# Kernel optimization log

Measured on AMD Instinct MI355X. Metric: run time of the kernel, lower is better.

Reference implementation:

```python
import jax, jax.numpy as jnp
import numpy as np

N = 4096; E = 65536; IN = 512; H = 256; QD = 256; NH = 8; HD = QD // NH
OUT = 10; L = 2; CT = 50


def _ln(x, g, b, eps=1e-5):
    mu = x.mean(-1, keepdims=True)
    var = ((x - mu) ** 2).mean(-1, keepdims=True)
    return (x - mu) * jax.lax.rsqrt(var + eps) * g + b


def _forward(x, edge_index, cell_types, Wi, bi, Wq, bq, Wk, bk, Wv, bv, Bc, cemb,
             Win, bin_p, Wo, bo, Wm1, bm1, Wm2, bm2, Wm3, bm3, ln_g, ln_b,
             Wc1, bc1, Wc2, bc2):
    src, tgt = edge_index[0], edge_index[1]
    h = jax.nn.relu(x @ Wi + bi)                      # [N, H] input projection
    # graph connectivity scattered into a dense mask (as in _create_attention_mask)
    mask = jnp.zeros((N, N), jnp.float32).at[src, tgt].set(1.0)
    for l in range(L):
        res = h
        Q = h @ Wq[l] + bq[l]                         # [N, QD]
        K = h @ Wk[l] + bk[l]
        V = h @ Wv[l] + bv[l]
        Q = Q @ Bc[l]                                 # biological constraint
        K = K @ Bc[l].T
        ce = cemb[l][cell_types]                      # [N, QD] cell-type embedding
        Q = Q + 0.1 * ce
        K = K + 0.1 * ce
        # dense graph-masked attention (entanglement matrix), applied to V
        scores = (Q @ K.T) / float(np.sqrt(QD))      # [N, N]
        scores = jnp.where(mask == 0.0, -1e9, scores)
        attn = jax.nn.softmax(scores, axis=-1)
        graph_att = attn @ V                          # [N, QD]
        # nn.MultiheadAttention(Q, K, V) entanglement layer (eval mode)
        q = (Q @ Win[l, :, :QD] + bin_p[l, :QD]).reshape(N, NH, HD)
        k = (K @ Win[l, :, QD:2 * QD] + bin_p[l, QD:2 * QD]).reshape(N, NH, HD)
        v = (V @ Win[l, :, 2 * QD:] + bin_p[l, 2 * QD:]).reshape(N, NH, HD)
        w = jax.nn.softmax(jnp.einsum('nhd,mhd->hnm', q, k) / float(np.sqrt(HD)), axis=-1)
        mha = jnp.einsum('hnm,mhd->nhd', w, v).reshape(N, QD) @ Wo[l] + bo[l]
        # edge gather -> message MLP -> scatter-add (PyG aggr='add', x_i=target, x_j=source)
        # quantum slot of the concat is zeros, so only the first 2H rows of Wm1 contribute
        m = jnp.concatenate([h[tgt], h[src]], axis=-1) @ Wm1[l, :2 * H] + bm1[l]
        m = jax.nn.relu(m)
        m = jax.nn.relu(m @ Wm2[l] + bm2[l])
        m = m @ Wm3[l] + bm3[l]                       # [E, H]
        agg = jax.ops.segment_sum(m, tgt, num_segments=N)
        h = _ln(res + agg + mha + graph_att, ln_g[l], ln_b[l])
    # graph-level readout: mean || max pooling -> classifier (hidden*2 -> hidden -> out)
    pooled = jnp.concatenate([h.mean(0), h.max(0)], axis=-1)   # [2H]
    z = jax.nn.relu(pooled @ Wc1 + bc1)
    return z @ Wc2 + bc2                              # [OUT]


def setup_inputs():
    ks = jax.random.split(jax.random.key(0), 40)
    s = 0.05
    p = lambda i, shape: jax.random.normal(ks[i], shape, jnp.float32) * s
    z = lambda shape: jnp.zeros(shape, jnp.float32)
    return {
        'x': jax.random.normal(ks[0], (N, IN), jnp.float32),
        'edge_index': jax.random.randint(ks[1], (2, E), 0, N),
        'cell_types': jax.random.randint(ks[2], (N,), 0, CT),
        'Wi': p(3, (IN, H)), 'bi': z((H,)),
        'Wq': p(4, (L, H, QD)), 'bq': z((L, QD)),
        'Wk': p(5, (L, H, QD)), 'bk': z((L, QD)),
        'Wv': p(6, (L, H, QD)), 'bv': z((L, QD)),
        'Bc': p(7, (L, QD, QD)),
        'cemb': p(8, (L, CT, QD)),
        'Win': p(9, (L, QD, 3 * QD)), 'bin_p': z((L, 3 * QD)),
        'Wo': p(10, (L, QD, QD)), 'bo': z((L, QD)),
        'Wm1': p(11, (L, 2 * H + QD, QD)), 'bm1': z((L, QD)),
        'Wm2': p(12, (L, QD, QD)), 'bm2': z((L, QD)),
        'Wm3': p(13, (L, QD, H)), 'bm3': z((L, H)),
        'ln_g': jnp.ones((L, H), jnp.float32), 'ln_b': z((L, H)),
        'Wc1': p(14, (2 * H, H)), 'bc1': z((H,)),
        'Wc2': p(15, (H, OUT)), 'bc2': z((OUT,)),
    }


def reference(x, edge_index, cell_types, Wi, bi, Wq, bq, Wk, bk, Wv, bv, Bc, cemb,
              Win, bin_p, Wo, bo, Wm1, bm1, Wm2, bm2, Wm3, bm3, ln_g, ln_b,
              Wc1, bc1, Wc2, bc2):
    return _forward(x, edge_index, cell_types, Wi, bi, Wq, bq, Wk, bk, Wv, bv, Bc, cemb,
                    Win, bin_p, Wo, bo, Wm1, bm1, Wm2, bm2, Wm3, bm3, ln_g, ln_b,
                    Wc1, bc1, Wc2, bc2)
```

## Files before the change

kernel.cpp:

```cpp
#include <hip/hip_runtime.h>
#include <hip/hip_bf16.h>

#define N_NODES 4096
#define E_EDGES 65536
#define IN_F    512
#define H_F     256
#define QD      256
#define NHEAD   8
#define HD      32
#define OUT_F   10
#define L_LAYERS 2
#define CT_N    50

enum { FLAG_RELU = 1, FLAG_ACCUM = 2, FLAG_WF32 = 4, FLAG_WB16 = 8 };

typedef __attribute__((ext_vector_type(8))) __bf16 bf16x8;
typedef __attribute__((ext_vector_type(4))) float f32x4;

union PU { bf16x8 v; __hip_bfloat16 h[8]; };

template<int BM, int BN, bool EDGE>
__global__ __launch_bounds__(256) void gemm_mfma(
    const __hip_bfloat16* __restrict__ A, int lda,
    const __hip_bfloat16* __restrict__ B, int ldb,
    float* __restrict__ Cf, __hip_bfloat16* __restrict__ Cb, int ldc,
    int K,
    const float* __restrict__ bias, const float* __restrict__ rowscale,
    const float* __restrict__ extra, const int* __restrict__ eidx, float esc,
    const int* __restrict__ tgtp, const int* __restrict__ srcp,
    const float* __restrict__ kbias,
    int flags)
{
    constexpr int WM = BM / 2, WN = BN / 2, MT = WM / 16, NT = WN / 16;
    constexpr int LDT = 40;
    __shared__ alignas(16) __hip_bfloat16 As[BM * LDT];
    __shared__ alignas(16) __hip_bfloat16 Bs[BN * LDT];

    const int tid = threadIdx.x;
    const int w = tid >> 6, lane = tid & 63, l16 = lane & 15, quad = lane >> 4;
    const int wm = w >> 1, wn = w & 1;
    const int bm = blockIdx.y * BM, bn = blockIdx.x * BN;

    f32x4 acc[MT][NT];
    #pragma unroll
    for (int i = 0; i < MT; ++i)
        #pragma unroll
        for (int j = 0; j < NT; ++j)
            #pragma unroll
            for (int r = 0; r < 4; ++r) acc[i][j][r] = 0.f;

    for (int k0 = 0; k0 < K; k0 += 32) {
        #pragma unroll
        for (int f = tid; f < BM * 4; f += 256) {
            int r = f >> 2, sg = f & 3;
            if (EDGE) {
                int i = bm + r;
                int tg = tgtp[i], sr = srcp[i];
                PU z1, z2, o;
                z1.v = *reinterpret_cast<const bf16x8*>(A + (size_t)tg * 512 + k0 + sg * 8);
                z2.v = *reinterpret_cast<const bf16x8*>(A + (size_t)sr * 512 + 256 + k0 + sg * 8);
                float4 b0 = *reinterpret_cast<const float4*>(kbias + k0 + sg * 8);
                float4 b1 = *reinterpret_cast<const float4*>(kbias + k0 + sg * 8 + 4);
                float bb[8] = {b0.x, b0.y, b0.z, b0.w, b1.x, b1.y, b1.z, b1.w};
                #pragma unroll
                for (int j = 0; j < 8; ++j) {
                    float v = __bfloat162float(z1.h[j]) + __bfloat162float(z2.h[j]) + bb[j];
                    o.h[j] = __float2bfloat16(fmaxf(v, 0.f));
                }
                *reinterpret_cast<bf16x8*>(&As[r * LDT + sg * 8]) = o.v;
            } else {
                *reinterpret_cast<uint4*>(&As[r * LDT + sg * 8]) =
                    *reinterpret_cast<const uint4*>(A + (size_t)(bm + r) * lda + k0 + sg * 8);
            }
        }
        #pragma unroll
        for (int f = tid; f < BN * 4; f += 256) {
            int r = f >> 2, sg = f & 3;
            *reinterpret_cast<uint4*>(&Bs[r * LDT + sg * 8]) =
                *reinterpret_cast<const uint4*>(B + (size_t)(bn + r) * ldb + k0 + sg * 8);
        }
        __syncthreads();
        bf16x8 af[MT], bfr[NT];
        #pragma unroll
        for (int mt = 0; mt < MT; ++mt)
            af[mt] = *reinterpret_cast<const bf16x8*>(&As[(wm * WM + mt * 16 + l16) * LDT + quad * 8]);
        #pragma unroll
        for (int nt = 0; nt < NT; ++nt)
            bfr[nt] = *reinterpret_cast<const bf16x8*>(&Bs[(wn * WN + nt * 16 + l16) * LDT + quad * 8]);
        #pragma unroll
        for (int mt = 0; mt < MT; ++mt)
            #pragma unroll
            for (int nt = 0; nt < NT; ++nt)
                acc[mt][nt] = __builtin_amdgcn_mfma_f32_16x16x32_bf16(af[mt], bfr[nt], acc[mt][nt], 0, 0, 0);
        __syncthreads();
    }

    #pragma unroll
    for (int mt = 0; mt < MT; ++mt) {
        #pragma unroll
        for (int nt = 0; nt < NT; ++nt) {
            int col = bn + wn * WN + nt * 16 + l16;
            #pragma unroll
            for (int r = 0; r < 4; ++r) {
                int row = bm + wm * WM + mt * 16 + quad * 4 + r;
                float v = acc[mt][nt][r];
                if (bias) {
                    float bv = bias[col];
                    if (rowscale) bv *= rowscale[row];
                    v += bv;
                }
                if (extra) v += esc * extra[(size_t)eidx[row] * QD + col];
                if (flags & FLAG_RELU) v = fmaxf(v, 0.f);
                size_t off = (size_t)row * ldc + col;
                if (flags & FLAG_ACCUM)     Cf[off] += v;
                else if (flags & FLAG_WF32) Cf[off] = v;
                if (flags & FLAG_WB16)      Cb[off] = __float2bfloat16(v);
            }
        }
    }
}

struct GSet { const __hip_bfloat16* A; int lda; const __hip_bfloat16* B;
              const float* bias; const float* rowscale;
              const float* extra; float esc; float cscale;
              __hip_bfloat16* C; float* Cf; int vtout; };
struct GPack3 { GSet s[3]; };

__global__ __launch_bounds__(256) void gemm_b3(GPack3 p, const int* __restrict__ eidx)
{
    GSet g = p.s[blockIdx.z];
    constexpr int LDT = 40;
    __shared__ alignas(16) __hip_bfloat16 As[64 * LDT];
    __shared__ alignas(16) __hip_bfloat16 Bs[64 * LDT];

    const int tid = threadIdx.x;
    const int w = tid >> 6, lane = tid & 63, l16 = lane & 15, quad = lane >> 4;
    const int wm = w >> 1, wn = w & 1;
    const int bm = blockIdx.y * 64, bn = blockIdx.x * 64;

    f32x4 acc[2][2];
    #pragma unroll
    for (int i = 0; i < 2; ++i)
        #pragma unroll
        for (int j = 0; j < 2; ++j)
            #pragma unroll
            for (int r = 0; r < 4; ++r) acc[i][j][r] = 0.f;

    for (int k0 = 0; k0 < 256; k0 += 32) {
        #pragma unroll
        for (int f = tid; f < 256; f += 256) {
            int r = f >> 2, sg = f & 3;
            *reinterpret_cast<uint4*>(&As[r * LDT + sg * 8]) =
                *reinterpret_cast<const uint4*>(g.A + (size_t)(bm + r) * g.lda + k0 + sg * 8);
            *reinterpret_cast<uint4*>(&Bs[r * LDT + sg * 8]) =
                *reinterpret_cast<const uint4*>(g.B + (size_t)(bn + r) * 256 + k0 + sg * 8);
        }
        __syncthreads();
        bf16x8 af[2], bfr[2];
        #pragma unroll
        for (int mt = 0; mt < 2; ++mt)
            af[mt] = *reinterpret_cast<const bf16x8*>(&As[(wm * 32 + mt * 16 + l16) * LDT + quad * 8]);
        #pragma unroll
        for (int nt = 0; nt < 2; ++nt)
            bfr[nt] = *reinterpret_cast<const bf16x8*>(&Bs[(wn * 32 + nt * 16 + l16) * LDT + quad * 8]);
        #pragma unroll
        for (int mt = 0; mt < 2; ++mt)
            #pragma unroll
            for (int nt = 0; nt < 2; ++nt)
                acc[mt][nt] = __builtin_amdgcn_mfma_f32_16x16x32_bf16(af[mt], bfr[nt], acc[mt][nt], 0, 0, 0);
        __syncthreads();
    }

    #pragma unroll
    for (int mt = 0; mt < 2; ++mt) {
        #pragma unroll
        for (int nt = 0; nt < 2; ++nt) {
            int col = bn + wn * 32 + nt * 16 + l16;
            #pragma unroll
            for (int r = 0; r < 4; ++r) {
                int row = bm + wm * 32 + mt * 16 + quad * 4 + r;
                float v = acc[mt][nt][r];
                if (g.bias) {
                    float bv = g.bias[col];
                    if (g.rowscale) bv *= g.rowscale[row];
                    v += bv;
                }
                if (g.extra) v += g.esc * g.extra[(size_t)eidx[row] * QD + col];
                v *= g.cscale;
                if (g.vtout)
                    g.C[(size_t)col * 4096 + row] = __float2bfloat16(v);
                else if (g.Cf)
                    g.Cf[(size_t)row * 256 + col] = v;
                else
                    g.C[(size_t)row * 256 + col] = __float2bfloat16(v);
            }
        }
    }
}

__global__ __launch_bounds__(256) void mha_flash5(
    const __hip_bfloat16* __restrict__ Qm,
    const __hip_bfloat16* __restrict__ Km,
    const __hip_bfloat16* __restrict__ Vt, __hip_bfloat16* __restrict__ Out)
{
    const int hh = blockIdx.y;
    const int tid = threadIdx.x;
    const int w = tid >> 6, lane = tid & 63, l16 = lane & 15, quad = lane >> 4;
    const int qb = blockIdx.x * 32;

    __shared__ float Osh[3][2][64][8];
    __shared__ float Lsh[3][2][16];

    const bf16x8 aq0 = *reinterpret_cast<const bf16x8*>(
        Qm + (size_t)(qb + l16) * 256 + hh * 32 + quad * 8);
    const bf16x8 aq1 = *reinterpret_cast<const bf16x8*>(
        Qm + (size_t)(qb + 16 + l16) * 256 + hh * 32 + quad * 8);
    const __hip_bfloat16* vb0 = Vt + (size_t)(hh * 32 + l16) * 4096;
    const __hip_bfloat16* vb1 = vb0 + (size_t)16 * 4096;
    const int rowoff = (l16 >> 2) * 8 + (l16 & 3);
    const f32x4 zero = {0.f, 0.f, 0.f, 0.f};

    f32x4 o00 = zero, o01 = zero, o10 = zero, o11 = zero;
    float l0 = 0.f, l1 = 0.f;

    const int kstart = w * 1024;
    for (int kt = 0; kt < 16; ++kt) {
        const int kbase = kstart + kt * 64;
        bf16x8 kf[4];
        #pragma unroll
        for (int c = 0; c < 2; ++c)
            #pragma unroll
            for (int st = 0; st < 2; ++st)
                kf[c * 2 + st] = *reinterpret_cast<const bf16x8*>(
                    Km + (size_t)(kbase + c * 32 + st * 4 + rowoff) * 256 + hh * 32 + quad * 8);
        bf16x8 v00 = *reinterpret_cast<const bf16x8*>(vb0 + kbase + quad * 8);
        bf16x8 v01 = *reinterpret_cast<const bf16x8*>(vb1 + kbase + quad * 8);
        bf16x8 v10 = *reinterpret_cast<const bf16x8*>(vb0 + kbase + 32 + quad * 8);
        bf16x8 v11 = *reinterpret_cast<const bf16x8*>(vb1 + kbase + 32 + quad * 8);

        {
            f32x4 s[4];
            #pragma unroll
            for (int i = 0; i < 4; ++i)
                s[i] = __builtin_amdgcn_mfma_f32_16x16x32_bf16(kf[i], aq0, zero, 0, 0, 0);
            PU p0, p1;
            float ls = 0.f;
            #pragma unroll
            for (int r = 0; r < 4; ++r) {
                float e0 = exp2f(s[0][r]), e1 = exp2f(s[1][r]);
                float e2 = exp2f(s[2][r]), e3 = exp2f(s[3][r]);
                ls += (e0 + e1) + (e2 + e3);
                p0.h[r] = __float2bfloat16(e0); p0.h[4 + r] = __float2bfloat16(e1);
                p1.h[r] = __float2bfloat16(e2); p1.h[4 + r] = __float2bfloat16(e3);
            }
            l0 += ls;
            o00 = __builtin_amdgcn_mfma_f32_16x16x32_bf16(v00, p0.v, o00, 0, 0, 0);
            o01 = __builtin_amdgcn_mfma_f32_16x16x32_bf16(v01, p0.v, o01, 0, 0, 0);
            o00 = __builtin_amdgcn_mfma_f32_16x16x32_bf16(v10, p1.v, o00, 0, 0, 0);
            o01 = __builtin_amdgcn_mfma_f32_16x16x32_bf16(v11, p1.v, o01, 0, 0, 0);
        }
        {
            f32x4 s[4];
            #pragma unroll
            for (int i = 0; i < 4; ++i)
                s[i] = __builtin_amdgcn_mfma_f32_16x16x32_bf16(kf[i], aq1, zero, 0, 0, 0);
            PU p0, p1;
            float ls = 0.f;
            #pragma unroll
            for (int r = 0; r < 4; ++r) {
                float e0 = exp2f(s[0][r]), e1 = exp2f(s[1][r]);
                float e2 = exp2f(s[2][r]), e3 = exp2f(s[3][r]);
                ls += (e0 + e1) + (e2 + e3);
                p0.h[r] = __float2bfloat16(e0); p0.h[4 + r] = __float2bfloat16(e1);
                p1.h[r] = __float2bfloat16(e2); p1.h[4 + r] = __float2bfloat16(e3);
            }
            l1 += ls;
            o10 = __builtin_amdgcn_mfma_f32_16x16x32_bf16(v00, p0.v, o10, 0, 0, 0);
            o11 = __builtin_amdgcn_mfma_f32_16x16x32_bf16(v01, p0.v, o11, 0, 0, 0);
            o10 = __builtin_amdgcn_mfma_f32_16x16x32_bf16(v10, p1.v, o10, 0, 0, 0);
            o11 = __builtin_amdgcn_mfma_f32_16x16x32_bf16(v11, p1.v, o11, 0, 0, 0);
        }
    }

    l0 += __shfl_xor(l0, 16); l0 += __shfl_xor(l0, 32);
    l1 += __shfl_xor(l1, 16); l1 += __shfl_xor(l1, 32);

    if (w > 0) {
        #pragma unroll
        for (int r = 0; r < 4; ++r) {
            Osh[w - 1][0][lane][r]     = o00[r];
            Osh[w - 1][0][lane][4 + r] = o01[r];
            Osh[w - 1][1][lane][r]     = o10[r];
            Osh[w - 1][1][lane][4 + r] = o11[r];
        }
        if (quad == 0) { Lsh[w - 1][0][l16] = l0; Lsh[w - 1][1][l16] = l1; }
    }
    __syncthreads();
    if (w == 0) {
        #pragma unroll
        for (int ww = 0; ww < 3; ++ww) {
            #pragma unroll
            for (int r = 0; r < 4; ++r) {
                o00[r] += Osh[ww][0][lane][r];
                o01[r] += Osh[ww][0][lane][4 + r];
                o10[r] += Osh[ww][1][lane][r];
                o11[r] += Osh[ww][1][lane][4 + r];
            }
            l0 += Lsh[ww][0][l16];
            l1 += Lsh[ww][1][l16];
        }
        {
            float inv = 1.f / l0;
            __hip_bfloat16* dst = Out + (size_t)(qb + l16) * 256 + hh * 32;
            #pragma unroll
            for (int r = 0; r < 4; ++r) {
                dst[quad * 4 + r]      = __float2bfloat16(o00[r] * inv);
                dst[16 + quad * 4 + r] = __float2bfloat16(o01[r] * inv);
            }
        }
        {
            float inv = 1.f / l1;
            __hip_bfloat16* dst = Out + (size_t)(qb + 16 + l16) * 256 + hh * 32;
            #pragma unroll
            for (int r = 0; r < 4; ++r) {
                dst[quad * 4 + r]      = __float2bfloat16(o10[r] * inv);
                dst[16 + quad * 4 + r] = __float2bfloat16(o11[r] * inv);
            }
        }
    }
}

__global__ __launch_bounds__(256) void build_mask(const int* __restrict__ src,
                                                  const int* __restrict__ tgt,
                                                  unsigned* __restrict__ mb)
{
    int e = blockIdx.x * 256 + threadIdx.x;
    if (e >= E_EDGES) return;
    atomicOr(mb + (size_t)src[e] * (N_NODES / 32) + (tgt[e] >> 5), 1u << (tgt[e] & 31));
}

__global__ __launch_bounds__(256) void csr_count(const int* __restrict__ tgt, int* __restrict__ cnt)
{
    int e = blockIdx.x * 256 + threadIdx.x;
    if (e < E_EDGES) atomicAdd(&cnt[tgt[e]], 1);
}

__global__ __launch_bounds__(1024) void csr_scan(const int* __restrict__ cnt, int* __restrict__ off,
                                                 int* __restrict__ cursor, float* __restrict__ degf)
{
    __shared__ int sh[1024];
    int t = threadIdx.x;
    int base = t * 4;
    int c0 = cnt[base], c1 = cnt[base + 1], c2 = cnt[base + 2], c3 = cnt[base + 3];
    int sum = c0 + c1 + c2 + c3;
    sh[t] = sum; __syncthreads();
    for (int d = 1; d < 1024; d <<= 1) {
        int v = (t >= d) ? sh[t - d] : 0;
        __syncthreads();
        sh[t] += v;
        __syncthreads();
    }
    int excl = sh[t] - sum;
    int o0 = excl, o1 = excl + c0, o2 = o1 + c1, o3 = o2 + c2;
    off[base] = o0; off[base + 1] = o1; off[base + 2] = o2; off[base + 3] = o3;
    cursor[base] = o0; cursor[base + 1] = o1; cursor[base + 2] = o2; cursor[base + 3] = o3;
    degf[base] = (float)c0; degf[base + 1] = (float)c1;
    degf[base + 2] = (float)c2; degf[base + 3] = (float)c3;
    if (t == 1023) off[4096] = sh[t];
}

__global__ __launch_bounds__(256) void csr_fill(const int* __restrict__ src, const int* __restrict__ tgt,
                                                int* __restrict__ cursor,
                                                int* __restrict__ srcp, int* __restrict__ tgtp)
{
    int e = blockIdx.x * 256 + threadIdx.x;
    if (e >= E_EDGES) return;
    int t = tgt[e];
    int pos = atomicAdd(&cursor[t], 1);
    srcp[pos] = src[e];
    tgtp[pos] = t;
}

__global__ __launch_bounds__(256) void seg_sum(const int* __restrict__ off,
                                               const __hip_bfloat16* __restrict__ M2,
                                               __hip_bfloat16* __restrict__ A3)
{
    int n = blockIdx.x, t = threadIdx.x;
    int b0 = off[n], b1 = off[n + 1];
    float s = 0.f;
    for (int i = b0; i < b1; ++i)
        s += __bfloat162float(M2[(size_t)i * 256 + t]);
    A3[(size_t)n * 256 + t] = __float2bfloat16(s);
}

__global__ __launch_bounds__(256) void sparse_attn(
    const __hip_bfloat16* __restrict__ Q, const __hip_bfloat16* __restrict__ K,
    const __hip_bfloat16* __restrict__ V, int vld,
    const unsigned* __restrict__ maskb, float* __restrict__ outb)
{
    int i = blockIdx.x, t = threadIdx.x;
    __shared__ float qsh[256];
    __shared__ int   nb[1024];
    __shared__ float sc[1024];
    __shared__ int   cnt;
    __shared__ float red[4];
    __shared__ float smax, ssum;
    if (t == 0) cnt = 0;
    qsh[t] = __bfloat162float(Q[(size_t)i * 256 + t]);
    __syncthreads();
    if (t < 128) {
        unsigned wv = maskb[(size_t)i * 128 + t];
        while (wv) {
            int b = __ffs(wv) - 1; wv &= wv - 1;
            int p = atomicAdd(&cnt, 1);
            nb[p] = t * 32 + b;
        }
    }
    __syncthreads();
    int deg = cnt;
    int wid = t >> 6, lane = t & 63;
    if (deg > 0) {
        for (int n = wid; n < deg; n += 4) {
            union { uint2 u; __hip_bfloat16 h[4]; } kv;
            kv.u = *reinterpret_cast<const uint2*>(K + (size_t)nb[n] * 256 + lane * 4);
            float s = qsh[lane*4+0] * __bfloat162float(kv.h[0]) + qsh[lane*4+1] * __bfloat162float(kv.h[1])
                    + qsh[lane*4+2] * __bfloat162float(kv.h[2]) + qsh[lane*4+3] * __bfloat162float(kv.h[3]);
            #pragma unroll
            for (int off = 32; off; off >>= 1) s += __shfl_xor(s, off);
            if (lane == 0) sc[n] = s * 0.0625f;
        }
        __syncthreads();
        float m = -3.4e38f;
        for (int n = t; n < deg; n += 256) m = fmaxf(m, sc[n]);
        #pragma unroll
        for (int off = 32; off; off >>= 1) m = fmaxf(m, __shfl_xor(m, off));
        if (lane == 0) red[wid] = m;
        __syncthreads();
        if (t == 0) smax = fmaxf(fmaxf(red[0], red[1]), fmaxf(red[2], red[3]));
        __syncthreads();
        float ls = 0.f;
        for (int n = t; n < deg; n += 256) { float e = __expf(sc[n] - smax); sc[n] = e; ls += e; }
        #pragma unroll
        for (int off = 32; off; off >>= 1) ls += __shfl_xor(ls, off);
        if (lane == 0) red[wid] = ls;
        __syncthreads();
        if (t == 0) ssum = red[0] + red[1] + red[2] + red[3];
        __syncthreads();
        float inv = 1.f / ssum;
        float o = 0.f;
        for (int n = 0; n < deg; ++n)
            o += sc[n] * __bfloat162float(V[(size_t)nb[n] * vld + t]);
        outb[(size_t)i * 256 + t] = o * inv;
    } else {
        float o = 0.f;
        for (int j = 0; j < N_NODES; ++j) o += __bfloat162float(V[(size_t)j * vld + t]);
        outb[(size_t)i * 256 + t] = o * (1.f / N_NODES);
    }
}

__global__ __launch_bounds__(256) void ln_kernel(float* __restrict__ h, __hip_bfloat16* __restrict__ h16,
                                                 const float* __restrict__ a1,
                                                 const float* __restrict__ a2,
                                                 const float* __restrict__ a3,
                                                 const float* __restrict__ g, const float* __restrict__ b)
{
    int row = blockIdx.x, t = threadIdx.x;
    __shared__ float red[256];
    size_t off = ((size_t)row << 8) + t;
    float v = h[off] + a1[off] + a2[off] + a3[off];
    red[t] = v; __syncthreads();
    for (int s = 128; s > 0; s >>= 1) { if (t < s) red[t] += red[t + s]; __syncthreads(); }
    float mu = red[0] * (1.f / 256.f); __syncthreads();
    float d = v - mu;
    red[t] = d * d; __syncthreads();
    for (int s = 128; s > 0; s >>= 1) { if (t < s) red[t] += red[t + s]; __syncthreads(); }
    float var = red[0] * (1.f / 256.f);
    float r = d * rsqrtf(var + 1e-5f) * g[t] + b[t];
    h[off] = r;
    h16[off] = __float2bfloat16(r);
}

__global__ __launch_bounds__(256) void colpool(const float* __restrict__ h, float* __restrict__ p)
{
    int c = blockIdx.x, t = threadIdx.x;
    __shared__ float rs[256], rm[256];
    float s = 0.f, m = -3.4e38f;
    for (int row = t; row < N_NODES; row += 256) {
        float v = h[((size_t)row << 8) + c];
        s += v; m = fmaxf(m, v);
    }
    rs[t] = s; rm[t] = m; __syncthreads();
    for (int st = 128; st > 0; st >>= 1) {
        if (t < st) { rs[t] += rs[t + st]; rm[t] = fmaxf(rm[t], rm[t + st]); }
        __syncthreads();
    }
    if (t == 0) { p[c] = rs[0] * (1.f / N_NODES); p[256 + c] = rm[0]; }
}

__global__ __launch_bounds__(256) void classifier(const float* __restrict__ pooled,
                                                  const float* __restrict__ Wc1, const float* __restrict__ bc1,
                                                  const float* __restrict__ Wc2, const float* __restrict__ bc2,
                                                  float* __restrict__ out)
{
    __shared__ float p[512];
    __shared__ float z[256];
    int t = threadIdx.x;
    p[t] = pooled[t]; p[256 + t] = pooled[256 + t];
    __syncthreads();
    float s = bc1[t];
    for (int k = 0; k < 512; ++k) s = fmaf(p[k], Wc1[k * 256 + t], s);
    z[t] = fmaxf(s, 0.f);
    __syncthreads();
    if (t < OUT_F) {
        float o = bc2[t];
        for (int j = 0; j < 256; ++j) o = fmaf(z[j], Wc2[j * OUT_F + t], o);
        out[t] = o;
    }
}

__global__ void concat_qkv_bias(const float* __restrict__ bq, const float* __restrict__ bk,
                                const float* __restrict__ bv, float* __restrict__ out)
{
    int l = blockIdx.x, t = threadIdx.x;
    float v = (t < 256) ? bq[l * 256 + t] : (t < 512) ? bk[l * 256 + t - 256] : bv[l * 256 + t - 512];
    out[l * 768 + t] = v;
}

struct CDesc { const float* s; __hip_bfloat16* d; int total; };
struct CPack { CDesc d[4]; };
__global__ __launch_bounds__(256) void convert_copy(CPack p)
{
    CDesc c = p.d[blockIdx.y];
    for (int i = blockIdx.x * 256 + threadIdx.x; i < c.total; i += gridDim.x * 256)
        c.d[i] = __float2bfloat16(c.s[i]);
}
struct TDesc { const float* s; __hip_bfloat16* d; int K, N, sld; };
struct TPack { TDesc d[25]; };
__global__ __launch_bounds__(256) void convert_t32(TPack p)
{
    TDesc c = p.d[blockIdx.z];
    int k0 = blockIdx.x * 32, n0 = blockIdx.y * 32;
    if (k0 >= c.K || n0 >= c.N) return;
    __shared__ float t[32][33];
    int tr = threadIdx.x >> 5, tc = threadIdx.x & 31;
    #pragma unroll
    for (int rr = 0; rr < 32; rr += 8)
        t[tc][tr + rr] = c.s[(size_t)(k0 + tr + rr) * c.sld + n0 + tc];
    __syncthreads();
    #pragma unroll
    for (int rr = 0; rr < 32; rr += 8)
        c.d[(size_t)(n0 + tr + rr) * c.K + k0 + tc] = __float2bfloat16(t[tr + rr][tc]);
}

template<int BM, int BN>
static void launchG(const __hip_bfloat16* A, int lda, const __hip_bfloat16* B, int ldb,
                    float* Cf, __hip_bfloat16* Cb, int ldc, int M, int Nn, int K,
                    const float* bias, const float* rowscale,
                    const float* extra, const int* eidx, float esc,
                    int flags, hipStream_t s)
{
    dim3 g(Nn / BN, M / BM);
    gemm_mfma<BM, BN, false><<<g, 256, 0, s>>>(A, lda, B, ldb, Cf, Cb, ldc, K, bias, rowscale,
                                               extra, eidx, esc, nullptr, nullptr, nullptr, flags);
}

extern "C" void kernel_launch(void* const* d_in, const int* in_sizes, int n_in,
                              void* d_out, int out_size, void* d_ws, size_t ws_size,
                              hipStream_t stream)
{
    const float* x    = (const float*)d_in[0];
    const int*   ei   = (const int*)d_in[1];
    const int*   ct   = (const int*)d_in[2];
    const float* Wi   = (const float*)d_in[3];
    const float* bi   = (const float*)d_in[4];
    const float* Wq   = (const float*)d_in[5];
    const float* bq   = (const float*)d_in[6];
    const float* Wk   = (const float*)d_in[7];
    const float* bk   = (const float*)d_in[8];
    const float* Wv   = (const float*)d_in[9];
    const float* bv   = (const float*)d_in[10];
    const float* Bc   = (const float*)d_in[11];
    const float* cemb = (const float*)d_in[12];
    const float* Win  = (const float*)d_in[13];
    const float* binp = (const float*)d_in[14];
    const float* Wo   = (const float*)d_in[15];
    const float* bo   = (const float*)d_in[16];
    const float* Wm1  = (const float*)d_in[17];
    const float* bm1  = (const float*)d_in[18];
    const float* Wm2  = (const float*)d_in[19];
    const float* bm2  = (const float*)d_in[20];
    const float* Wm3  = (const float*)d_in[21];
    const float* bm3  = (const float*)d_in[22];
    const float* lng  = (const float*)d_in[23];
    const float* lnb  = (const float*)d_in[24];
    const float* Wc1  = (const float*)d_in[25];
    const float* bc1  = (const float*)d_in[26];
    const float* Wc2  = (const float*)d_in[27];
    const float* bc2  = (const float*)d_in[28];

    const int* src = ei;
    const int* tgt = ei + E_EDGES;

    char* wp = (char*)d_ws;
    auto alloc = [&](size_t bytes) { char* r = wp; wp += (bytes + 255) & ~(size_t)255; return r; };
    const size_t NH = (size_t)N_NODES * 256;
    float* h      = (float*)alloc(NH * 4);
    float* a1     = (float*)alloc(NH * 4);
    float* a2     = (float*)alloc(NH * 4);
    float* a3     = (float*)alloc(NH * 4);
    float* pooled = (float*)alloc(512 * 4);
    float* bqkv   = (float*)alloc(2 * 768 * 4);
    float* degf   = (float*)alloc(N_NODES * 4);
    __hip_bfloat16* x16 = (__hip_bfloat16*)alloc((size_t)N_NODES * 512 * 2);
    __hip_bfloat16* h16 = (__hip_bfloat16*)alloc(NH * 2);
    __hip_bfloat16* Ta  = (__hip_bfloat16*)alloc((size_t)N_NODES * 768 * 2);
    __hip_bfloat16* Qb  = (__hip_bfloat16*)alloc(NH * 2);
    __hip_bfloat16* Kb  = (__hip_bfloat16*)alloc(NH * 2);
    __hip_bfloat16* Tq  = (__hip_bfloat16*)alloc(NH * 2);
    __hip_bfloat16* Tk  = (__hip_bfloat16*)alloc(NH * 2);
    __hip_bfloat16* Vt  = (__hip_bfloat16*)alloc(NH * 2);
    __hip_bfloat16* Z12 = (__hip_bfloat16*)alloc((size_t)N_NODES * 512 * 2);
    __hip_bfloat16* M216= (__hip_bfloat16*)alloc((size_t)E_EDGES * 256 * 2);
    __hip_bfloat16* A3  = (__hip_bfloat16*)alloc(NH * 2);
    __hip_bfloat16* Wi_t= (__hip_bfloat16*)alloc((size_t)256 * 512 * 2);
    __hip_bfloat16* WB[2][10];
    for (int l = 0; l < 2; ++l) {
        WB[l][0] = (__hip_bfloat16*)alloc(3 * 65536 * 2);
        for (int m = 1; m < 7; ++m) WB[l][m] = (__hip_bfloat16*)alloc(65536 * 2);
        WB[l][7] = (__hip_bfloat16*)alloc(2 * 65536 * 2);
        WB[l][8] = (__hip_bfloat16*)alloc(65536 * 2);
        WB[l][9] = (__hip_bfloat16*)alloc(65536 * 2);
    }
    unsigned* maskb = (unsigned*)alloc((size_t)N_NODES * 128 * 4);
    int* cnt    = (int*)alloc(N_NODES * 4);
    int* cursor = (int*)alloc(N_NODES * 4);
    int* off    = (int*)alloc((N_NODES + 1) * 4);
    int* srcp   = (int*)alloc(E_EDGES * 4);
    int* tgtp   = (int*)alloc(E_EDGES * 4);

    CPack cp; int ndc = 0;
    TPack tp; int ndt = 0;
    auto addT = [&](const float* s, __hip_bfloat16* d, int K, int N, int sld) { tp.d[ndt++] = {s, d, K, N, sld}; };
    auto addC = [&](const float* s, __hip_bfloat16* d, int total) { cp.d[ndc++] = {s, d, total}; };
    addC(x, x16, N_NODES * 512);
    addT(Wi, Wi_t, 512, 256, 256);
    for (int l = 0; l < 2; ++l) {
        const float* Wq_l  = Wq + (size_t)l * 65536;
        const float* Wk_l  = Wk + (size_t)l * 65536;
        const float* Wv_l  = Wv + (size_t)l * 65536;
        const float* Bc_l  = Bc + (size_t)l * 65536;
        const float* Win_l = Win + (size_t)l * 256 * 768;
        const float* Wo_l  = Wo + (size_t)l * 65536;
        const float* Wm1_l = Wm1 + (size_t)l * (2 * H_F + QD) * QD;
        const float* Wm2_l = Wm2 + (size_t)l * 65536;
        const float* Wm3_l = Wm3 + (size_t)l * 65536;
        addT(Wq_l, WB[l][0],          256, 256, 256);
        addT(Wk_l, WB[l][0] + 65536,  256, 256, 256);
        addT(Wv_l, WB[l][0] + 131072, 256, 256, 256);
        addT(Bc_l, WB[l][1], 256, 256, 256);
        addC(Bc_l, WB[l][2], 65536);
        addT(Win_l,        WB[l][3], 256, 256, 768);
        addT(Win_l + 256,  WB[l][4], 256, 256, 768);
        addT(Win_l + 512,  WB[l][5], 256, 256, 768);
        addT(Wo_l, WB[l][6], 256, 256, 256);
        addT(Wm1_l,             WB[l][7],         256, 256, 256);
        addT(Wm1_l + 256 * 256, WB[l][7] + 65536, 256, 256, 256);
        addT(Wm2_l, WB[l][8], 256, 256, 256);
        addT(Wm3_l, WB[l][9], 256, 256, 256);
    }
    convert_copy<<<dim3(256, ndc), 256, 0, stream>>>(cp);
    convert_t32<<<dim3(16, 8, ndt), 256, 0, stream>>>(tp);
    concat_qkv_bias<<<2, 768, 0, stream>>>(bq, bk, bv, bqkv);

    hipMemsetAsync(maskb, 0, (size_t)N_NODES * 128 * 4, stream);
    hipMemsetAsync(cnt, 0, N_NODES * 4, stream);
    build_mask<<<E_EDGES / 256, 256, 0, stream>>>(src, tgt, maskb);
    csr_count<<<E_EDGES / 256, 256, 0, stream>>>(tgt, cnt);
    csr_scan<<<1, 1024, 0, stream>>>(cnt, off, cursor, degf);
    csr_fill<<<E_EDGES / 256, 256, 0, stream>>>(src, tgt, cursor, srcp, tgtp);

    launchG<64, 64>(x16, 512, Wi_t, 512, h, h16, 256, N_NODES, 256, 512,
                    bi, nullptr, nullptr, nullptr, 0.f, FLAG_RELU | FLAG_WF32 | FLAG_WB16, stream);

    const float QSCALE = 0.25507693f;

    for (int l = 0; l < L_LAYERS; ++l) {
        const float* ce_l  = cemb + (size_t)l * CT_N * QD;
        const float* bin_l = binp + l * 3 * QD;
        const float* bo_l  = bo + l * QD;
        const float* bm1_l = bm1 + l * QD;
        const float* bm2_l = bm2 + l * QD;
        const float* bm3_l = bm3 + l * H_F;
        const float* lng_l = lng + l * H_F;
        const float* lnb_l = lnb + l * H_F;

        launchG<64, 64>(h16, 256, WB[l][0], 256, nullptr, Ta, 768, N_NODES, 768, 256,
                        bqkv + l * 768, nullptr, nullptr, nullptr, 0.f, FLAG_WB16, stream);
        {
            GPack3 gp;
            gp.s[0] = {Ta,       768, WB[l][1], nullptr, nullptr, ce_l, 0.1f, 1.0f, Qb, nullptr, 0};
            gp.s[1] = {Ta + 256, 768, WB[l][2], nullptr, nullptr, ce_l, 0.1f, 1.0f, Kb, nullptr, 0};
            gemm_b3<<<dim3(4, 64, 2), 256, 0, stream>>>(gp, ct);
        }

        sparse_attn<<<N_NODES, 256, 0, stream>>>(Qb, Kb, Ta + 512, 768, maskb, a1);

        {
            GPack3 gp;
            gp.s[0] = {Qb,       256, WB[l][3], bin_l,          nullptr, nullptr, 0.f, QSCALE, Tq, nullptr, 0};
            gp.s[1] = {Kb,       256, WB[l][4], bin_l + QD,     nullptr, nullptr, 0.f, 1.0f,   Tk, nullptr, 0};
            gp.s[2] = {Ta + 512, 768, WB[l][5], bin_l + 2 * QD, nullptr, nullptr, 0.f, 1.0f,   Vt, nullptr, 1};
            gemm_b3<<<dim3(4, 64, 3), 256, 0, stream>>>(gp, ct);
        }

        mha_flash5<<<dim3(128, NHEAD), 256, 0, stream>>>(Tq, Tk, Vt, Qb);

        launchG<64, 64>(h16, 256, WB[l][7], 256, nullptr, Z12, 512, N_NODES, 512, 256,
                        nullptr, nullptr, nullptr, nullptr, 0.f, FLAG_WB16, stream);
        {
            dim3 g(256 / 128, E_EDGES / 128);
            gemm_mfma<128, 128, true><<<g, 256, 0, stream>>>(
                Z12, 512, WB[l][8], 256, nullptr, M216, 256, 256,
                bm2_l, nullptr, nullptr, nullptr, 0.f, tgtp, srcp, bm1_l,
                FLAG_RELU | FLAG_WB16);
        }
        seg_sum<<<N_NODES, 256, 0, stream>>>(off, M216, A3);

        {
            GPack3 gp;
            gp.s[0] = {Qb, 256, WB[l][6], bo_l,  nullptr, nullptr, 0.f, 1.0f, nullptr, a2, 0};
            gp.s[1] = {A3, 256, WB[l][9], bm3_l, degf,    nullptr, 0.f, 1.0f, nullptr, a3, 0};
            gemm_b3<<<dim3(4, 64, 2), 256, 0, stream>>>(gp, ct);
        }

        ln_kernel<<<N_NODES, 256, 0, stream>>>(h, h16, a1, a2, a3, lng_l, lnb_l);
    }

    colpool<<<H_F, 256, 0, stream>>>(h, pooled);
    classifier<<<1, 256, 0, stream>>>(pooled, Wc1, bc1, Wc2, bc2, (float*)d_out);
}
```

Baseline: 618.1 us.

## Fold chained linear projections into precomposed weights and batch all per-layer GEMMs

Precomposes weight products on device (Wq·Bc, Wk·Bc^T, then those times the Win slices, plus matching biases and cell-embedding projections), so Q, K, V, the MHA q/k/v and the message-MLP first layer all become single GEMMs from h. These eight GEMMs run in one batched launch instead of a chain of three dependent GEMM stages. The MHA flash kernel also prefetches the next K/V tile into registers. This removes serial GEMM launches and intermediate round-trips, at the cost of a naive fp32 weight-composition kernel and different bf16 rounding of the fused weights.

```diff
diff --git a/kernel.cpp b/kernel.cpp
--- a/kernel.cpp
+++ b/kernel.cpp
@@ -26,7 +26,6 @@
     float* __restrict__ Cf, __hip_bfloat16* __restrict__ Cb, int ldc,
     int K,
     const float* __restrict__ bias, const float* __restrict__ rowscale,
-    const float* __restrict__ extra, const int* __restrict__ eidx, float esc,
     const int* __restrict__ tgtp, const int* __restrict__ srcp,
     const float* __restrict__ kbias,
     int flags)
@@ -109,7 +108,6 @@
                     if (rowscale) bv *= rowscale[row];
                     v += bv;
                 }
-                if (extra) v += esc * extra[(size_t)eidx[row] * QD + col];
                 if (flags & FLAG_RELU) v = fmaxf(v, 0.f);
                 size_t off = (size_t)row * ldc + col;
                 if (flags & FLAG_ACCUM)     Cf[off] += v;
@@ -123,10 +121,10 @@
 struct GSet { const __hip_bfloat16* A; int lda; const __hip_bfloat16* B;
               const float* bias; const float* rowscale;
               const float* extra; float esc; float cscale;
-              __hip_bfloat16* C; float* Cf; int vtout; };
-struct GPack3 { GSet s[3]; };
-
-__global__ __launch_bounds__(256) void gemm_b3(GPack3 p, const int* __restrict__ eidx)
+              __hip_bfloat16* C; float* Cf; int vtout; int ldc; int coloff; };
+struct GPack { GSet s[8]; };
+
+__global__ __launch_bounds__(256) void gemm_bz(GPack p, const int* __restrict__ eidx)
 {
     GSet g = p.s[blockIdx.z];
     constexpr int LDT = 40;
@@ -175,30 +173,51 @@
     for (int mt = 0; mt < 2; ++mt) {
         #pragma unroll
         for (int nt = 0; nt < 2; ++nt) {
-            int col = bn + wn * 32 + nt * 16 + l16;
+            int colL = bn + wn * 32 + nt * 16 + l16;
             #pragma unroll
             for (int r = 0; r < 4; ++r) {
                 int row = bm + wm * 32 + mt * 16 + quad * 4 + r;
                 float v = acc[mt][nt][r];
                 if (g.bias) {
-                    float bv = g.bias[col];
+                    float bv = g.bias[colL];
                     if (g.rowscale) bv *= g.rowscale[row];
                     v += bv;
                 }
-                if (g.extra) v += g.esc * g.extra[(size_t)eidx[row] * QD + col];
+                if (g.extra) v += g.esc * g.extra[(size_t)eidx[row] * QD + colL];
                 v *= g.cscale;
                 if (g.vtout)
-                    g.C[(size_t)col * 4096 + row] = __float2bfloat16(v);
+                    g.C[(size_t)colL * 4096 + row] = __float2bfloat16(v);
                 else if (g.Cf)
-                    g.Cf[(size_t)row * 256 + col] = v;
+                    g.Cf[(size_t)row * g.ldc + g.coloff + colL] = v;
                 else
-                    g.C[(size_t)row * 256 + col] = __float2bfloat16(v);
+                    g.C[(size_t)row * g.ldc + g.coloff + colL] = __float2bfloat16(v);
             }
         }
     }
 }
 
-__global__ __launch_bounds__(256) void mha_flash5(
+struct FDesc { const float* A; int lda; const float* B; int ldb; int tb;
+               const float* bias; float* C; int M, N, K; };
+struct FPack { FDesc d[16]; };
+
+__global__ __launch_bounds__(256) void fgemm(FPack p)
+{
+    FDesc c = p.d[blockIdx.z];
+    int el = blockIdx.x * 256 + threadIdx.x;
+    if (el >= c.M * c.N) return;
+    int m = el / c.N, n = el - m * c.N;
+    float acc = c.bias ? c.bias[n] : 0.f;
+    if (c.tb) {
+        for (int k = 0; k < c.K; ++k)
+            acc += c.A[(size_t)m * c.lda + k] * c.B[(size_t)n * c.ldb + k];
+    } else {
+        for (int k = 0; k < c.K; ++k)
+            acc += c.A[(size_t)m * c.lda + k] * c.B[(size_t)k * c.ldb + n];
+    }
+    c.C[(size_t)m * c.N + n] = acc;
+}
+
+__global__ __launch_bounds__(256) void mha_flash6(
     const __hip_bfloat16* __restrict__ Qm,
     const __hip_bfloat16* __restrict__ Km,
     const __hip_bfloat16* __restrict__ Vt, __hip_bfloat16* __restrict__ Out)
@@ -224,19 +243,31 @@
     float l0 = 0.f, l1 = 0.f;
 
     const int kstart = w * 1024;
+    bf16x8 kf[4], vf[4];
+    #pragma unroll
+    for (int c = 0; c < 2; ++c)
+        #pragma unroll
+        for (int st = 0; st < 2; ++st)
+            kf[c * 2 + st] = *reinterpret_cast<const bf16x8*>(
+                Km + (size_t)(kstart + c * 32 + st * 4 + rowoff) * 256 + hh * 32 + quad * 8);
+    vf[0] = *reinterpret_cast<const bf16x8*>(vb0 + kstart + quad * 8);
+    vf[1] = *reinterpret_cast<const bf16x8*>(vb1 + kstart + quad * 8);
+    vf[2] = *reinterpret_cast<const bf16x8*>(vb0 + kstart + 32 + quad * 8);
+    vf[3] = *reinterpret_cast<const bf16x8*>(vb1 + kstart + 32 + quad * 8);
+
     for (int kt = 0; kt < 16; ++kt) {
-        const int kbase = kstart + kt * 64;
-        bf16x8 kf[4];
+        const int nb = kstart + ((kt + 1) & 15) * 64;
+        bf16x8 nkf[4], nvf[4];
         #pragma unroll
         for (int c = 0; c < 2; ++c)
             #pragma unroll
             for (int st = 0; st < 2; ++st)
-                kf[c * 2 + st] = *reinterpret_cast<const bf16x8*>(
-                    Km + (size_t)(kbase + c * 32 + st * 4 + rowoff) * 256 + hh * 32 + quad * 8);
-        bf16x8 v00 = *reinterpret_cast<const bf16x8*>(vb0 + kbase + quad * 8);
-        bf16x8 v01 = *reinterpret_cast<const bf16x8*>(vb1 + kbase + quad * 8);
-        bf16x8 v10 = *reinterpret_cast<const bf16x8*>(vb0 + kbase + 32 + quad * 8);
-        bf16x8 v11 = *reinterpret_cast<const bf16x8*>(vb1 + kbase + 32 + quad * 8);
+                nkf[c * 2 + st] = *reinterpret_cast<const bf16x8*>(
+                    Km + (size_t)(nb + c * 32 + st * 4 + rowoff) * 256 + hh * 32 + quad * 8);
+        nvf[0] = *reinterpret_cast<const bf16x8*>(vb0 + nb + quad * 8);
+        nvf[1] = *reinterpret_cast<const bf16x8*>(vb1 + nb + quad * 8);
+        nvf[2] = *reinterpret_cast<const bf16x8*>(vb0 + nb + 32 + quad * 8);
+        nvf[3] = *reinterpret_cast<const bf16x8*>(vb1 + nb + 32 + quad * 8);
 
         {
             f32x4 s[4];
@@ -254,10 +285,10 @@
                 p1.h[r] = __float2bfloat16(e2); p1.h[4 + r] = __float2bfloat16(e3);
             }
             l0 += ls;
-            o00 = __builtin_amdgcn_mfma_f32_16x16x32_bf16(v00, p0.v, o00, 0, 0, 0);
-            o01 = __builtin_amdgcn_mfma_f32_16x16x32_bf16(v01, p0.v, o01, 0, 0, 0);
-            o00 = __builtin_amdgcn_mfma_f32_16x16x32_bf16(v10, p1.v, o00, 0, 0, 0);
-            o01 = __builtin_amdgcn_mfma_f32_16x16x32_bf16(v11, p1.v, o01, 0, 0, 0);
+            o00 = __builtin_amdgcn_mfma_f32_16x16x32_bf16(vf[0], p0.v, o00, 0, 0, 0);
+            o01 = __builtin_amdgcn_mfma_f32_16x16x32_bf16(vf[1], p0.v, o01, 0, 0, 0);
+            o00 = __builtin_amdgcn_mfma_f32_16x16x32_bf16(vf[2], p1.v, o00, 0, 0, 0);
+            o01 = __builtin_amdgcn_mfma_f32_16x16x32_bf16(vf[3], p1.v, o01, 0, 0, 0);
         }
         {
             f32x4 s[4];
@@ -275,11 +306,13 @@
                 p1.h[r] = __float2bfloat16(e2); p1.h[4 + r] = __float2bfloat16(e3);
             }
             l1 += ls;
-            o10 = __builtin_amdgcn_mfma_f32_16x16x32_bf16(v00, p0.v, o10, 0, 0, 0);
-            o11 = __builtin_amdgcn_mfma_f32_16x16x32_bf16(v01, p0.v, o11, 0, 0, 0);
-            o10 = __builtin_amdgcn_mfma_f32_16x16x32_bf16(v10, p1.v, o10, 0, 0, 0);
-            o11 = __builtin_amdgcn_mfma_f32_16x16x32_bf16(v11, p1.v, o11, 0, 0, 0);
-        }
+            o10 = __builtin_amdgcn_mfma_f32_16x16x32_bf16(vf[0], p0.v, o10, 0, 0, 0);
+            o11 = __builtin_amdgcn_mfma_f32_16x16x32_bf16(vf[1], p0.v, o11, 0, 0, 0);
+            o10 = __builtin_amdgcn_mfma_f32_16x16x32_bf16(vf[2], p1.v, o10, 0, 0, 0);
+            o11 = __builtin_amdgcn_mfma_f32_16x16x32_bf16(vf[3], p1.v, o11, 0, 0, 0);
+        }
+        #pragma unroll
+        for (int i = 0; i < 4; ++i) { kf[i] = nkf[i]; vf[i] = nvf[i]; }
     }
 
     l0 += __shfl_xor(l0, 16); l0 += __shfl_xor(l0, 32);
@@ -518,16 +551,8 @@
     }
 }
 
-__global__ void concat_qkv_bias(const float* __restrict__ bq, const float* __restrict__ bk,
-                                const float* __restrict__ bv, float* __restrict__ out)
-{
-    int l = blockIdx.x, t = threadIdx.x;
-    float v = (t < 256) ? bq[l * 256 + t] : (t < 512) ? bk[l * 256 + t - 256] : bv[l * 256 + t - 512];
-    out[l * 768 + t] = v;
-}
-
 struct CDesc { const float* s; __hip_bfloat16* d; int total; };
-struct CPack { CDesc d[4]; };
+struct CPack { CDesc d[2]; };
 __global__ __launch_bounds__(256) void convert_copy(CPack p)
 {
     CDesc c = p.d[blockIdx.y];
@@ -535,7 +560,7 @@
         c.d[i] = __float2bfloat16(c.s[i]);
 }
 struct TDesc { const float* s; __hip_bfloat16* d; int K, N, sld; };
-struct TPack { TDesc d[25]; };
+struct TPack { TDesc d[23]; };
 __global__ __launch_bounds__(256) void convert_t32(TPack p)
 {
     TDesc c = p.d[blockIdx.z];
@@ -550,18 +575,6 @@
     #pragma unroll
     for (int rr = 0; rr < 32; rr += 8)
         c.d[(size_t)(n0 + tr + rr) * c.K + k0 + tc] = __float2bfloat16(t[tr + rr][tc]);
-}
-
-template<int BM, int BN>
-static void launchG(const __hip_bfloat16* A, int lda, const __hip_bfloat16* B, int ldb,
-                    float* Cf, __hip_bfloat16* Cb, int ldc, int M, int Nn, int K,
-                    const float* bias, const float* rowscale,
-                    const float* extra, const int* eidx, float esc,
-                    int flags, hipStream_t s)
-{
-    dim3 g(Nn / BN, M / BM);
-    gemm_mfma<BM, BN, false><<<g, 256, 0, s>>>(A, lda, B, ldb, Cf, Cb, ldc, K, bias, rowscale,
-                                               extra, eidx, esc, nullptr, nullptr, nullptr, flags);
 }
 
 extern "C" void kernel_launch(void* const* d_in, const int* in_sizes, int n_in,
@@ -609,13 +622,12 @@
     float* a2     = (float*)alloc(NH * 4);
     float* a3     = (float*)alloc(NH * 4);
     float* pooled = (float*)alloc(512 * 4);
-    float* bqkv   = (float*)alloc(2 * 768 * 4);
     float* degf   = (float*)alloc(N_NODES * 4);
     __hip_bfloat16* x16 = (__hip_bfloat16*)alloc((size_t)N_NODES * 512 * 2);
     __hip_bfloat16* h16 = (__hip_bfloat16*)alloc(NH * 2);
-    __hip_bfloat16* Ta  = (__hip_bfloat16*)alloc((size_t)N_NODES * 768 * 2);
     __hip_bfloat16* Qb  = (__hip_bfloat16*)alloc(NH * 2);
     __hip_bfloat16* Kb  = (__hip_bfloat16*)alloc(NH * 2);
+    __hip_bfloat16* Vb  = (__hip_bfloat16*)alloc(NH * 2);
     __hip_bfloat16* Tq  = (__hip_bfloat16*)alloc(NH * 2);
     __hip_bfloat16* Tk  = (__hip_bfloat16*)alloc(NH * 2);
     __hip_bfloat16* Vt  = (__hip_bfloat16*)alloc(NH * 2);
@@ -623,14 +635,21 @@
     __hip_bfloat16* M216= (__hip_bfloat16*)alloc((size_t)E_EDGES * 256 * 2);
     __hip_bfloat16* A3  = (__hip_bfloat16*)alloc(NH * 2);
     __hip_bfloat16* Wi_t= (__hip_bfloat16*)alloc((size_t)256 * 512 * 2);
-    __hip_bfloat16* WB[2][10];
+    float *Wqc_f[2], *Wkc_f[2], *Wqm_f[2], *Wkm_f[2], *Wvm_f[2];
+    float *bqc[2], *bkc[2], *bqm[2], *bkm[2], *bvm[2], *ceq2[2], *cek2[2];
     for (int l = 0; l < 2; ++l) {
-        WB[l][0] = (__hip_bfloat16*)alloc(3 * 65536 * 2);
-        for (int m = 1; m < 7; ++m) WB[l][m] = (__hip_bfloat16*)alloc(65536 * 2);
-        WB[l][7] = (__hip_bfloat16*)alloc(2 * 65536 * 2);
-        WB[l][8] = (__hip_bfloat16*)alloc(65536 * 2);
-        WB[l][9] = (__hip_bfloat16*)alloc(65536 * 2);
-    }
+        Wqc_f[l] = (float*)alloc(65536 * 4); Wkc_f[l] = (float*)alloc(65536 * 4);
+        Wqm_f[l] = (float*)alloc(65536 * 4); Wkm_f[l] = (float*)alloc(65536 * 4);
+        Wvm_f[l] = (float*)alloc(65536 * 4);
+        bqc[l] = (float*)alloc(256 * 4); bkc[l] = (float*)alloc(256 * 4);
+        bqm[l] = (float*)alloc(256 * 4); bkm[l] = (float*)alloc(256 * 4);
+        bvm[l] = (float*)alloc(256 * 4);
+        ceq2[l] = (float*)alloc(CT_N * 256 * 4); cek2[l] = (float*)alloc(CT_N * 256 * 4);
+    }
+    __hip_bfloat16* WB[2][11];
+    for (int l = 0; l < 2; ++l)
+        for (int m = 0; m < 11; ++m)
+            WB[l][m] = (__hip_bfloat16*)alloc(65536 * 2);
     unsigned* maskb = (unsigned*)alloc((size_t)N_NODES * 128 * 4);
     int* cnt    = (int*)alloc(N_NODES * 4);
     int* cursor = (int*)alloc(N_NODES * 4);
@@ -638,39 +657,60 @@
     int* srcp   = (int*)alloc(E_EDGES * 4);
     int* tgtp   = (int*)alloc(E_EDGES * 4);
 
-    CPack cp; int ndc = 0;
-    TPack tp; int ndt = 0;
-    auto addT = [&](const float* s, __hip_bfloat16* d, int K, int N, int sld) { tp.d[ndt++] = {s, d, K, N, sld}; };
-    auto addC = [&](const float* s, __hip_bfloat16* d, int total) { cp.d[ndc++] = {s, d, total}; };
-    addC(x, x16, N_NODES * 512);
-    addT(Wi, Wi_t, 512, 256, 256);
+    CPack cp; cp.d[0] = {x, x16, N_NODES * 512};
+    convert_copy<<<dim3(256, 1), 256, 0, stream>>>(cp);
+
+    FPack f1; int n1 = 0;
+    FPack f2; int n2 = 0;
     for (int l = 0; l < 2; ++l) {
         const float* Wq_l  = Wq + (size_t)l * 65536;
         const float* Wk_l  = Wk + (size_t)l * 65536;
         const float* Wv_l  = Wv + (size_t)l * 65536;
         const float* Bc_l  = Bc + (size_t)l * 65536;
         const float* Win_l = Win + (size_t)l * 256 * 768;
+        const float* ce_l  = cemb + (size_t)l * CT_N * QD;
+        const float* bq_l  = bq + l * 256;
+        const float* bk_l  = bk + l * 256;
+        const float* bv_l  = bv + l * 256;
+        const float* bin_l = binp + l * 768;
+        f1.d[n1++] = {Wq_l, 256, Bc_l, 256, 0, nullptr, Wqc_f[l], 256, 256, 256};
+        f1.d[n1++] = {Wk_l, 256, Bc_l, 256, 1, nullptr, Wkc_f[l], 256, 256, 256};
+        f1.d[n1++] = {bq_l, 256, Bc_l, 256, 0, nullptr, bqc[l], 1, 256, 256};
+        f1.d[n1++] = {bk_l, 256, Bc_l, 256, 1, nullptr, bkc[l], 1, 256, 256};
+        f2.d[n2++] = {Wqc_f[l], 256, Win_l,       768, 0, nullptr, Wqm_f[l], 256, 256, 256};
+        f2.d[n2++] = {Wkc_f[l], 256, Win_l + 256, 768, 0, nullptr, Wkm_f[l], 256, 256, 256};
+        f2.d[n2++] = {Wv_l,     256, Win_l + 512, 768, 0, nullptr, Wvm_f[l], 256, 256, 256};
+        f2.d[n2++] = {ce_l,     256, Win_l,       768, 0, nullptr, ceq2[l], CT_N, 256, 256};
+        f2.d[n2++] = {ce_l,     256, Win_l + 256, 768, 0, nullptr, cek2[l], CT_N, 256, 256};
+        f2.d[n2++] = {bqc[l],   256, Win_l,       768, 0, bin_l,       bqm[l], 1, 256, 256};
+        f2.d[n2++] = {bkc[l],   256, Win_l + 256, 768, 0, bin_l + 256, bkm[l], 1, 256, 256};
+        f2.d[n2++] = {bv_l,     256, Win_l + 512, 768, 0, bin_l + 512, bvm[l], 1, 256, 256};
+    }
+    fgemm<<<dim3(256, 1, n1), 256, 0, stream>>>(f1);
+    fgemm<<<dim3(256, 1, n2), 256, 0, stream>>>(f2);
+
+    TPack tp; int ndt = 0;
+    auto addT = [&](const float* s, __hip_bfloat16* d, int K, int N, int sld) { tp.d[ndt++] = {s, d, K, N, sld}; };
+    addT(Wi, Wi_t, 512, 256, 256);
+    for (int l = 0; l < 2; ++l) {
+        const float* Wv_l  = Wv + (size_t)l * 65536;
         const float* Wo_l  = Wo + (size_t)l * 65536;
         const float* Wm1_l = Wm1 + (size_t)l * (2 * H_F + QD) * QD;
         const float* Wm2_l = Wm2 + (size_t)l * 65536;
         const float* Wm3_l = Wm3 + (size_t)l * 65536;
-        addT(Wq_l, WB[l][0],          256, 256, 256);
-        addT(Wk_l, WB[l][0] + 65536,  256, 256, 256);
-        addT(Wv_l, WB[l][0] + 131072, 256, 256, 256);
-        addT(Bc_l, WB[l][1], 256, 256, 256);
-        addC(Bc_l, WB[l][2], 65536);
-        addT(Win_l,        WB[l][3], 256, 256, 768);
-        addT(Win_l + 256,  WB[l][4], 256, 256, 768);
-        addT(Win_l + 512,  WB[l][5], 256, 256, 768);
-        addT(Wo_l, WB[l][6], 256, 256, 256);
-        addT(Wm1_l,             WB[l][7],         256, 256, 256);
-        addT(Wm1_l + 256 * 256, WB[l][7] + 65536, 256, 256, 256);
-        addT(Wm2_l, WB[l][8], 256, 256, 256);
-        addT(Wm3_l, WB[l][9], 256, 256, 256);
-    }
-    convert_copy<<<dim3(256, ndc), 256, 0, stream>>>(cp);
+        addT(Wqc_f[l], WB[l][0], 256, 256, 256);
+        addT(Wkc_f[l], WB[l][1], 256, 256, 256);
+        addT(Wqm_f[l], WB[l][2], 256, 256, 256);
+        addT(Wkm_f[l], WB[l][3], 256, 256, 256);
+        addT(Wvm_f[l], WB[l][4], 256, 256, 256);
+        addT(Wv_l,     WB[l][5], 256, 256, 256);
+        addT(Wo_l,     WB[l][6], 256, 256, 256);
+        addT(Wm1_l,             WB[l][7], 256, 256, 256);
+        addT(Wm1_l + 256 * 256, WB[l][8], 256, 256, 256);
+        addT(Wm2_l,    WB[l][9],  256, 256, 256);
+        addT(Wm3_l,    WB[l][10], 256, 256, 256);
+    }
     convert_t32<<<dim3(16, 8, ndt), 256, 0, stream>>>(tp);
-    concat_qkv_bias<<<2, 768, 0, stream>>>(bq, bk, bv, bqkv);
 
     hipMemsetAsync(maskb, 0, (size_t)N_NODES * 128 * 4, stream);
     hipMemsetAsync(cnt, 0, N_NODES * 4, stream);
@@ -679,58 +719,49 @@
     csr_scan<<<1, 1024, 0, stream>>>(cnt, off, cursor, degf);
     csr_fill<<<E_EDGES / 256, 256, 0, stream>>>(src, tgt, cursor, srcp, tgtp);
 
-    launchG<64, 64>(x16, 512, Wi_t, 512, h, h16, 256, N_NODES, 256, 512,
-                    bi, nullptr, nullptr, nullptr, 0.f, FLAG_RELU | FLAG_WF32 | FLAG_WB16, stream);
+    gemm_mfma<64, 64, false><<<dim3(4, 64), 256, 0, stream>>>(
+        x16, 512, Wi_t, 512, h, h16, 256, 512,
+        bi, nullptr, nullptr, nullptr, nullptr, FLAG_RELU | FLAG_WF32 | FLAG_WB16);
 
     const float QSCALE = 0.25507693f;
 
     for (int l = 0; l < L_LAYERS; ++l) {
         const float* ce_l  = cemb + (size_t)l * CT_N * QD;
-        const float* bin_l = binp + l * 3 * QD;
         const float* bo_l  = bo + l * QD;
         const float* bm1_l = bm1 + l * QD;
         const float* bm2_l = bm2 + l * QD;
         const float* bm3_l = bm3 + l * H_F;
         const float* lng_l = lng + l * H_F;
         const float* lnb_l = lnb + l * H_F;
-
-        launchG<64, 64>(h16, 256, WB[l][0], 256, nullptr, Ta, 768, N_NODES, 768, 256,
-                        bqkv + l * 768, nullptr, nullptr, nullptr, 0.f, FLAG_WB16, stream);
+        const float* bv_l  = bv + l * 256;
+
         {
-            GPack3 gp;
-            gp.s[0] = {Ta,       768, WB[l][1], nullptr, nullptr, ce_l, 0.1f, 1.0f, Qb, nullptr, 0};
-            gp.s[1] = {Ta + 256, 768, WB[l][2], nullptr, nullptr, ce_l, 0.1f, 1.0f, Kb, nullptr, 0};
-            gemm_b3<<<dim3(4, 64, 2), 256, 0, stream>>>(gp, ct);
-        }
-
-        sparse_attn<<<N_NODES, 256, 0, stream>>>(Qb, Kb, Ta + 512, 768, maskb, a1);
+            GPack gp;
+            gp.s[0] = {h16, 256, WB[l][0], bqc[l], nullptr, ce_l,    0.1f, 1.0f,   Qb,  nullptr, 0, 256, 0};
+            gp.s[1] = {h16, 256, WB[l][1], bkc[l], nullptr, ce_l,    0.1f, 1.0f,   Kb,  nullptr, 0, 256, 0};
+            gp.s[2] = {h16, 256, WB[l][5], bv_l,   nullptr, nullptr, 0.f,  1.0f,   Vb,  nullptr, 0, 256, 0};
+            gp.s[3] = {h16, 256, WB[l][2], bqm[l], nullptr, ceq2[l], 0.1f, QSCALE, Tq,  nullptr, 0, 256, 0};
+            gp.s[4] = {h16, 256, WB[l][3], bkm[l], nullptr, cek2[l], 0.1f, 1.0f,   Tk,  nullptr, 0, 256, 0};
+            gp.s[5] = {h16, 256, WB[l][4], bvm[l], nullptr, nullptr, 0.f,  1.0f,   Vt,  nullptr, 1, 256, 0};
+            gp.s[6] = {h16, 256, WB[l][7], nullptr, nullptr, nullptr, 0.f, 1.0f,   Z12, nullptr, 0, 512, 0};
+            gp.s[7] = {h16, 256, WB[l][8], nullptr, nullptr, nullptr, 0.f, 1.0f,   Z12, nullptr, 0, 512, 256};
+            gemm_bz<<<dim3(4, 64, 8), 256, 0, stream>>>(gp, ct);
+        }
+
+        sparse_attn<<<N_NODES, 256, 0, stream>>>(Qb, Kb, Vb, 256, maskb, a1);
+
+        mha_flash6<<<dim3(128, NHEAD), 256, 0, stream>>>(Tq, Tk, Vt, Qb);
+
+        gemm_mfma<128, 128, true><<<dim3(2, E_EDGES / 128), 256, 0, stream>>>(
+            Z12, 512, WB[l][9], 256, nullptr, M216, 256, 256,
+            bm2_l, nullptr, tgtp, srcp, bm1_l, FLAG_RELU | FLAG_WB16);
+        seg_sum<<<N_NODES, 256, 0, stream>>>(off, M216, A3);
 
         {
-            GPack3 gp;
-            gp.s[0] = {Qb,       256, WB[l][3], bin_l,          nullptr, nullptr, 0.f, QSCALE, Tq, nullptr, 0};
-            gp.s[1] = {Kb,       256, WB[l][4], bin_l + QD,     nullptr, nullptr, 0.f, 1.0f,   Tk, nullptr, 0};
-            gp.s[2] = {Ta + 512, 768, WB[l][5], bin_l + 2 * QD, nullptr, nullptr, 0.f, 1.0f,   Vt, nullptr, 1};
-            gemm_b3<<<dim3(4, 64, 3), 256, 0, stream>>>(gp, ct);
-        }
-
-        mha_flash5<<<dim3(128, NHEAD), 256, 0, stream>>>(Tq, Tk, Vt, Qb);
-
-        launchG<64, 64>(h16, 256, WB[l][7], 256, nullptr, Z12, 512, N_NODES, 512, 256,
-                        nullptr, nullptr, nullptr, nullptr, 0.f, FLAG_WB16, stream);
-        {
-            dim3 g(256 / 128, E_EDGES / 128);
-            gemm_mfma<128, 128, true><<<g, 256, 0, stream>>>(
-                Z12, 512, WB[l][8], 256, nullptr, M216, 256, 256,
-                bm2_l, nullptr, nullptr, nullptr, 0.f, tgtp, srcp, bm1_l,
-                FLAG_RELU | FLAG_WB16);
-        }
-        seg_sum<<<N_NODES, 256, 0, stream>>>(off, M216, A3);
-
-        {
-            GPack3 gp;
-            gp.s[0] = {Qb, 256, WB[l][6], bo_l,  nullptr, nullptr, 0.f, 1.0f, nullptr, a2, 0};
-            gp.s[1] = {A3, 256, WB[l][9], bm3_l, degf,    nullptr, 0.f, 1.0f, nullptr, a3, 0};
-            gemm_b3<<<dim3(4, 64, 2), 256, 0, stream>>>(gp, ct);
+            GPack gp;
+            gp.s[0] = {Qb, 256, WB[l][6],  bo_l,  nullptr, nullptr, 0.f, 1.0f, nullptr, a2, 0, 256, 0};
+            gp.s[1] = {A3, 256, WB[l][10], bm3_l, degf,    nullptr, 0.f, 1.0f, nullptr, a3, 0, 256, 0};
+            gemm_bz<<<dim3(4, 64, 2), 256, 0, stream>>>(gp, ct);
         }
 
         ln_kernel<<<N_NODES, 256, 0, stream>>>(h, h16, a1, a2, a3, lng_l, lnb_l);
```

New measurement: 828.3 us. +34.0%, slower.
